# Optimization experiments

Hardware: AMD Instinct MI355X
Metric: run time of the kernel (lower is better)

The kernel has to match this reference:

```python
import jax, jax.numpy as jnp
import numpy as np

N = 10000      # nodes per graph-batch
E = 160000     # edges
G = 128        # number of graphs (segments)


def gcn_conv(x, edge_index, W, b, n):
    """PyG GCNConv with normalize=True, add_self_loops=True.
    x: [n, in], W: [in, out], b: [out], edge_index: [2, e]."""
    loops = jnp.arange(n, dtype=edge_index.dtype)
    src = jnp.concatenate([edge_index[0], loops])
    dst = jnp.concatenate([edge_index[1], loops])
    deg = jnp.zeros((n,), x.dtype).at[dst].add(1.0)          # in-degree incl. self-loops
    dinv = jnp.where(deg > 0, jax.lax.rsqrt(deg), 0.0)
    norm = dinv[src] * dinv[dst]                              # [e+n]
    h = x @ W                                                 # dense transform first
    out = jax.ops.segment_sum(norm[:, None] * h[src], dst, num_segments=n)
    return out + b


def global_max_pool(z, batch, g):
    p = jax.ops.segment_max(z, batch, num_segments=g)
    return jnp.where(jnp.isneginf(p), 0.0, p)  # guard empty segments


def setup_inputs() -> dict:
    key = jax.random.key(0)
    ks = jax.random.split(key, 24)

    def w(k, i, o):
        return (jax.random.normal(k, (i, o), jnp.float32) / np.sqrt(i)).astype(jnp.float32)

    inp = {
        "x_s": jax.random.normal(ks[0], (N, 128), jnp.float32),
        "x_t": jax.random.normal(ks[1], (N, 128), jnp.float32),
        "edge_index_s": jax.random.randint(ks[2], (2, E), 0, N, dtype=jnp.int32),
        "edge_index_t": jax.random.randint(ks[3], (2, E), 0, N, dtype=jnp.int32),
        "xs_batch": jnp.sort(jax.random.randint(ks[4], (N,), 0, G, dtype=jnp.int32)),
        "xt_batch": jnp.sort(jax.random.randint(ks[5], (N,), 0, G, dtype=jnp.int32)),
        # encoder GCNConvs (128 -> 512)
        "W_enc1": w(ks[6], 128, 512), "b_enc1": jnp.zeros((512,), jnp.float32),
        "W_enc2": w(ks[7], 128, 512), "b_enc2": jnp.zeros((512,), jnp.float32),
        # branch-1 GCNConvs
        "W_r1g1": w(ks[8], 512, 1024), "b_r1g1": jnp.zeros((1024,), jnp.float32),
        "W_r1g2": w(ks[9], 1024, 2048), "b_r1g2": jnp.zeros((2048,), jnp.float32),
        # branch-2 GCNConvs
        "W_r2g1": w(ks[10], 512, 1024), "b_r2g1": jnp.zeros((1024,), jnp.float32),
        "W_r2g2": w(ks[11], 1024, 2048), "b_r2g2": jnp.zeros((2048,), jnp.float32),
        # MLP head
        "W_l1": w(ks[12], 2048, 1024), "b_l1": jnp.zeros((1024,), jnp.float32),
        "W_l2": w(ks[13], 1024, 1317), "b_l2": jnp.zeros((1317,), jnp.float32),
    }
    return inp


def reference(x_s, x_t, W_enc1, b_enc1, W_enc2, b_enc2,
              W_r1g1, b_r1g1, W_r1g2, b_r1g2,
              W_r2g1, b_r2g1, W_r2g2, b_r2g2,
              W_l1, b_l1, W_l2, b_l2,
              edge_index_s, edge_index_t, xs_batch, xt_batch):
    # branch 1 (source graphs)
    enc_r1 = gcn_conv(x_s, edge_index_s, W_enc1, b_enc1, N)
    z_r1 = jax.nn.relu(gcn_conv(enc_r1, edge_index_s, W_r1g1, b_r1g1, N))
    z_r1 = jax.nn.relu(gcn_conv(z_r1, edge_index_s, W_r1g2, b_r1g2, N))
    # branch 2 (target graphs)
    enc_r2 = gcn_conv(x_t, edge_index_t, W_enc2, b_enc2, N)
    z_r2 = jax.nn.relu(gcn_conv(enc_r2, edge_index_t, W_r2g1, b_r2g1, N))
    z_r2 = jax.nn.relu(gcn_conv(z_r2, edge_index_t, W_r2g2, b_r2g2, N))
    # global max pool per graph, then MLP head
    z = global_max_pool(z_r1, xs_batch, G) + global_max_pool(z_r2, xt_batch, G)  # [G, 2048]
    z = jax.nn.relu(z @ W_l1 + b_l1)
    z = z @ W_l2 + b_l2                                                          # [G, 1317]
    return (z, jax.nn.sigmoid(z))
```

## Files before the change

kernel.cpp:

```cpp
#include <hip/hip_runtime.h>
#include <cstdint>
#include <cstddef>


#define NN 10000
#define NNP2 10240
#define MT2 20480
#define NB2 640
#define NE 160000
#define NG 128

typedef short bf16x8 __attribute__((ext_vector_type(8)));
typedef float f32x4 __attribute__((ext_vector_type(4)));

__device__ __forceinline__ unsigned short f2bf(float x) {
  unsigned u = __float_as_uint(x);
  u += 0x7FFFu + ((u >> 16) & 1u);
  return (unsigned short)(u >> 16);
}
__device__ __forceinline__ float bf2f(unsigned short h) {
  return __uint_as_float(((unsigned)h) << 16);
}
__device__ __forceinline__ void fma4(float4& d, float s, const float4& u) {
  d.x = fmaf(s, u.x, d.x);
  d.y = fmaf(s, u.y, d.y);
  d.z = fmaf(s, u.z, d.z);
  d.w = fmaf(s, u.w, d.w);
}

#define GLOAD_LDS16(gp, lp)                                                  \
  __builtin_amdgcn_global_load_lds(                                          \
      (const __attribute__((address_space(1))) void*)(gp),                   \
      (__attribute__((address_space(3))) void*)(lp), 16, 0, 0)


__global__ void k_count2(const int* __restrict__ eis, const int* __restrict__ eit,
                         int* __restrict__ cnt) {
  int i = blockIdx.x * blockDim.x + threadIdx.x;
  if (i >= 2 * NE) return;
  int d;
  if (i < NE) d = eis[NE + i];
  else        d = eit[NE + (i - NE)] + NNP2;
  atomicAdd(&cnt[d], 1);
}

__global__ void k_scan(const int* __restrict__ cnt, int* __restrict__ row_ptr,
                       int* __restrict__ cursor, float* __restrict__ dinv) {
  __shared__ int part[256];
  __shared__ int partex[257];
  int t = threadIdx.x;
  const int n = MT2;
  const int CH = n / 256;
  int base = t * CH;
  int s = 0;
  for (int i = 0; i < CH; ++i) s += cnt[base + i];
  part[t] = s;
  __syncthreads();
  if (t == 0) {
    int acc = 0;
    for (int i = 0; i < 256; ++i) { partex[i] = acc; acc += part[i]; }
    partex[256] = acc;
  }
  __syncthreads();
  int acc = partex[t];
  for (int i = 0; i < CH; ++i) {
    int idx = base + i;
    row_ptr[idx] = acc;
    cursor[idx]  = acc;
    dinv[idx] = rsqrtf((float)cnt[idx] + 1.0f);
    acc += cnt[idx];
  }
  if (t == 255) row_ptr[n] = partex[256];
}

__global__ void k_scatter2(const int* __restrict__ eis, const int* __restrict__ eit,
                           int* __restrict__ cursor, int* __restrict__ csr_src) {
  int i = blockIdx.x * blockDim.x + threadIdx.x;
  if (i >= 2 * NE) return;
  int s, d;
  if (i < NE) { s = eis[i]; d = eis[NE + i]; }
  else { int j = i - NE; s = eit[j] + NNP2; d = eit[NE + j] + NNP2; }
  int pos = atomicAdd(&cursor[d], 1);
  csr_src[pos] = s;
}

template <int NCH, bool DUAL>
__global__ __launch_bounds__(256) void k_agg_x(
    const float* __restrict__ in0, const float* __restrict__ in1,
    unsigned short* __restrict__ Ah, unsigned short* __restrict__ Al,
    const int* __restrict__ row_ptr, const int* __restrict__ csr_src,
    const float* __restrict__ dinv) {
  constexpr int F4TOT = NCH * 8;
  const int bid = blockIdx.x;
  const int xcd = bid & 7;
  const int seq = bid >> 3;
  int chunk, nodeblk;
  if constexpr (NCH >= 8) {
    int phase = seq / NB2;
    nodeblk = seq - phase * NB2;
    chunk = phase * 8 + xcd;
  } else {
    chunk = xcd >> 1;
    nodeblk = (seq << 1) | (xcd & 1);
  }
  const int t = threadIdx.x;
  const int node = nodeblk * 32 + (t >> 3);
  const int f4 = chunk * 8 + (t & 7);

  size_t o = (size_t)node * F4TOT + f4;
  ushort4* oh = (ushort4*)Ah + o;
  ushort4* ol = (ushort4*)Al + o;
  int local = (node < NNP2) ? node : (node - NNP2);
  if (local >= NN) {
    *oh = make_ushort4(0, 0, 0, 0);
    *ol = make_ushort4(0, 0, 0, 0);
    return;
  }
  const float4* i0 = (const float4*)in0;
  const float4* i1 = (const float4*)in1;
  auto rowp = [&](int g) -> const float4* {
    if (DUAL)
      return (g < NNP2) ? (i0 + (size_t)g * F4TOT)
                        : (i1 + (size_t)(g - NNP2) * F4TOT);
    return i0 + (size_t)g * F4TOT;
  };

  float di = dinv[node];
  float sw = di * di;
  float4 v = rowp(node)[f4];
  float4 acc;
  acc.x = sw * v.x; acc.y = sw * v.y; acc.z = sw * v.z; acc.w = sw * v.w;

  const int e0 = row_ptr[node], e1 = row_ptr[node + 1];
  int e = e0;
  for (; e + 4 <= e1; e += 4) {
    int s0 = csr_src[e], s1 = csr_src[e + 1];
    int s2 = csr_src[e + 2], s3 = csr_src[e + 3];
    float4 u0 = rowp(s0)[f4];
    float4 u1 = rowp(s1)[f4];
    float4 u2 = rowp(s2)[f4];
    float4 u3 = rowp(s3)[f4];
    float w0 = dinv[s0] * di, w1 = dinv[s1] * di;
    float w2 = dinv[s2] * di, w3 = dinv[s3] * di;
    fma4(acc, w0, u0);
    fma4(acc, w1, u1);
    fma4(acc, w2, u2);
    fma4(acc, w3, u3);
  }
  for (; e < e1; ++e) {
    int s = csr_src[e];
    float4 u = rowp(s)[f4];
    fma4(acc, dinv[s] * di, u);
  }

  ushort4 h, l;
  h.x = f2bf(acc.x); l.x = f2bf(acc.x - bf2f(h.x));
  h.y = f2bf(acc.y); l.y = f2bf(acc.y - bf2f(h.y));
  h.z = f2bf(acc.z); l.z = f2bf(acc.z - bf2f(h.z));
  h.w = f2bf(acc.w); l.w = f2bf(acc.w - bf2f(h.w));
  *oh = h;
  *ol = l;
}

__global__ __launch_bounds__(256) void k_wsplit2(
    const float* __restrict__ W0, unsigned short* __restrict__ H0,
    unsigned short* __restrict__ L0,
    const float* __restrict__ W1, unsigned short* __restrict__ H1,
    unsigned short* __restrict__ L1, int K, int N) {
  const float* W = blockIdx.z ? W1 : W0;
  unsigned short* Ht = blockIdx.z ? H1 : H0;
  unsigned short* Lt = blockIdx.z ? L1 : L0;
  __shared__ float tile[32][33];
  int nb = blockIdx.x * 32, kb = blockIdx.y * 32;
  int tx = threadIdx.x & 31, ty = threadIdx.x >> 5;
#pragma unroll
  for (int r = ty; r < 32; r += 8)
    tile[r][tx] = W[(size_t)(kb + r) * N + nb + tx];
  __syncthreads();
#pragma unroll
  for (int r = ty; r < 32; r += 8) {
    float x = tile[tx][r];
    unsigned short h = f2bf(x);
    unsigned short lo = f2bf(x - bf2f(h));
    size_t o = (size_t)(nb + r) * K + kb + tx;
    Ht[o] = h;
    Lt[o] = lo;
  }
}

template <bool RELU, int GX>
__global__ __launch_bounds__(256) void k_mgemm(
    const unsigned short* __restrict__ Ah, const unsigned short* __restrict__ Al,
    const unsigned short* __restrict__ Bh_a, const unsigned short* __restrict__ Bl_a,
    const unsigned short* __restrict__ Bh_b, const unsigned short* __restrict__ Bl_b,
    const float* __restrict__ bias_a, const float* __restrict__ bias_b,
    float* __restrict__ C, int N, int K) {
  __shared__ char smem[65536];
  const int t = threadIdx.x;
  const int w = t >> 6, l = t & 63;

  const int bid = blockIdx.x;
  const int bn_ = bid & (GX - 1), bm_ = bid / GX;
  const int bm = bm_ * 128, bn = bn_ * 128;
  const bool sec = bm >= NNP2;
  const unsigned short* Bh = sec ? Bh_b : Bh_a;
  const unsigned short* Bl = sec ? Bl_b : Bl_a;
  const float* bias = sec ? bias_b : bias_a;

  const int wr = w >> 1, wc = w & 1;

  f32x4 acc[4][4] = {};

  const unsigned short* g0 = (w == 0) ? Ah : (w == 1) ? Al : (w == 2) ? Bh : Bl;
  const int rb = (w < 2) ? bm : bn;
  const unsigned short* gbase = g0 + (size_t)(rb + (l & 15)) * K + ((l >> 4) * 8);
  const int sdoff = w * 8192 + l * 16;
  const int saoff = wr * 4096 + l * 16;
  const int sboff = 16384 + wc * 4096 + l * 16;

  const int nt = K >> 5;

#define STAGE(kt, b)                                                         \
  {                                                                          \
    const unsigned short* gk = gbase + ((kt) << 5);                          \
    char* sd = smem + (b)*32768 + sdoff;                                     \
    _Pragma("unroll") for (int s = 0; s < 8; ++s)                            \
        GLOAD_LDS16(gk + (size_t)s * 16 * K, sd + s * 1024);                 \
  }

  STAGE(0, 0)

  for (int kt = 0; kt < nt; ++kt) {
    const int cur = kt & 1;
    if (kt + 1 < nt) {
      STAGE(kt + 1, cur ^ 1)
      asm volatile("s_waitcnt vmcnt(8)" ::: "memory");
    } else {
      asm volatile("s_waitcnt vmcnt(0)" ::: "memory");
    }
    __builtin_amdgcn_sched_barrier(0);
    __builtin_amdgcn_s_barrier();

    const char* sA = smem + cur * 32768 + saoff;
    const char* sB = smem + cur * 32768 + sboff;
    bf16x8 a[4][2], b[4][2];
#pragma unroll
    for (int i = 0; i < 4; ++i) {
      a[i][0] = *(const bf16x8*)(sA + i * 1024);
      a[i][1] = *(const bf16x8*)(sA + 8192 + i * 1024);
    }
#pragma unroll
    for (int j = 0; j < 4; ++j) {
      b[j][0] = *(const bf16x8*)(sB + j * 1024);
      b[j][1] = *(const bf16x8*)(sB + 8192 + j * 1024);
    }
    asm volatile("s_waitcnt lgkmcnt(0)" ::: "memory");
    __builtin_amdgcn_sched_barrier(0);
    __builtin_amdgcn_s_barrier();

    __builtin_amdgcn_s_setprio(1);
#pragma unroll
    for (int i = 0; i < 4; ++i)
#pragma unroll
      for (int j = 0; j < 4; ++j) {
        acc[i][j] = __builtin_amdgcn_mfma_f32_16x16x32_bf16(a[i][0], b[j][0], acc[i][j], 0, 0, 0);
        acc[i][j] = __builtin_amdgcn_mfma_f32_16x16x32_bf16(a[i][0], b[j][1], acc[i][j], 0, 0, 0);
        acc[i][j] = __builtin_amdgcn_mfma_f32_16x16x32_bf16(a[i][1], b[j][0], acc[i][j], 0, 0, 0);
      }
    __builtin_amdgcn_s_setprio(0);
  }
#undef STAGE

  const int r0 = bm + wr * 64 + ((l >> 4) << 2);
  const int c0 = bn + wc * 64 + (l & 15);
#pragma unroll
  for (int j = 0; j < 4; ++j) {
    const int col = c0 + j * 16;
    const float bv = bias[col];
#pragma unroll
    for (int i = 0; i < 4; ++i) {
      const int row = r0 + i * 16;
#pragma unroll
      for (int r = 0; r < 4; ++r) {
        float v = acc[i][j][r] + bv;
        if (RELU) v = fmaxf(v, 0.f);
        C[(size_t)(row + r) * N + col] = v;
      }
    }
  }
}

__global__ __launch_bounds__(512, 2) void k_mgemm3(
    const unsigned short* __restrict__ Ah, const unsigned short* __restrict__ Al,
    const unsigned short* __restrict__ Bh_a, const unsigned short* __restrict__ Bl_a,
    const unsigned short* __restrict__ Bh_b, const unsigned short* __restrict__ Bl_b,
    const float* __restrict__ bias_a, const float* __restrict__ bias_b,
    const int* __restrict__ bs, const int* __restrict__ bt,
    float* __restrict__ P2, int N, int K) {
  __shared__ char smem[131072];
  const int t = threadIdx.x;
  const int w = t >> 6, l = t & 63;
  const int bid = blockIdx.x;
  const int bn_ = bid & 7, bm_ = bid >> 3;
  const int bm = bm_ * 256, bn = bn_ * 256;
  const bool sec = bm >= NNP2;
  const unsigned short* Bh = sec ? Bh_b : Bh_a;
  const unsigned short* Bl = sec ? Bl_b : Bl_a;
  const float* bias = sec ? bias_b : bias_a;
  const int* batch = sec ? bt : bs;
  float* P2g = P2 + (sec ? (size_t)NG * 2048 : 0);
  const int lbase = bm - (sec ? NNP2 : 0);

  const int wr = w >> 2, wc = w & 3;

  f32x4 acc[8][4] = {};

  const int part = w >> 1, half = w & 1;
  const unsigned short* gmat = (part == 0) ? Ah : (part == 1) ? Al
                             : (part == 2) ? Bh : Bl;
  const int rb = ((part < 2) ? bm : bn) + half * 128;
  const unsigned short* gsbase = gmat + (size_t)(rb + (l & 15)) * K + ((l >> 4) * 8);
  const int sdoff = part * 16384 + half * 8192 + l * 16;

  const int saoff = (wr * 8) * 1024 + l * 16;
  const int sboff = 32768 + (wc * 4) * 1024 + l * 16;

  const int nt = K >> 5;

#define STAGE3(kt, b)                                                        \
  {                                                                          \
    _Pragma("unroll") for (int c = 0; c < 8; ++c)                            \
        GLOAD_LDS16(gsbase + (size_t)c * 16 * K + ((kt) << 5),               \
                    smem + (b)*65536 + sdoff + c * 1024);                    \
  }

  STAGE3(0, 0)

  for (int kt = 0; kt < nt; ++kt) {
    const int cur = kt & 1;
    if (kt + 1 < nt) {
      STAGE3(kt + 1, cur ^ 1)
      asm volatile("s_waitcnt vmcnt(8)" ::: "memory");
    } else {
      asm volatile("s_waitcnt vmcnt(0)" ::: "memory");
    }
    __builtin_amdgcn_sched_barrier(0);
    __builtin_amdgcn_s_barrier();

    const char* base = smem + cur * 65536;
    bf16x8 bh[4], blo[4], ah[8], alo[8];
#pragma unroll
    for (int j = 0; j < 4; ++j) {
      bh[j]  = *(const bf16x8*)(base + sboff + j * 1024);
      blo[j] = *(const bf16x8*)(base + sboff + 16384 + j * 1024);
    }
#pragma unroll
    for (int i = 0; i < 8; ++i) {
      ah[i]  = *(const bf16x8*)(base + saoff + i * 1024);
      alo[i] = *(const bf16x8*)(base + saoff + 16384 + i * 1024);
    }
    asm volatile("s_waitcnt lgkmcnt(0)" ::: "memory");
    __builtin_amdgcn_sched_barrier(0);
    __builtin_amdgcn_s_barrier();

    __builtin_amdgcn_s_setprio(1);
#pragma unroll
    for (int i = 0; i < 8; ++i)
#pragma unroll
      for (int j = 0; j < 4; ++j) {
        acc[i][j] = __builtin_amdgcn_mfma_f32_16x16x32_bf16(ah[i], bh[j], acc[i][j], 0, 0, 0);
        acc[i][j] = __builtin_amdgcn_mfma_f32_16x16x32_bf16(ah[i], blo[j], acc[i][j], 0, 0, 0);
        acc[i][j] = __builtin_amdgcn_mfma_f32_16x16x32_bf16(alo[i], bh[j], acc[i][j], 0, 0, 0);
      }
    __builtin_amdgcn_s_setprio(0);
  }
#undef STAGE3

  const int r0l = lbase + wr * 128 + ((l >> 4) << 2);
  const int c0 = bn + wc * 64 + (l & 15);
#pragma unroll
  for (int j = 0; j < 4; ++j) {
    const int col = c0 + j * 16;
    const float bv = bias[col];
    float* Pcol = P2g + col;
#pragma unroll
    for (int i = 0; i < 8; ++i) {
      const int rl = r0l + i * 16;
      if (rl >= NN) continue;
      float v0 = fmaxf(acc[i][j][0] + bv, 0.f);
      float v1 = fmaxf(acc[i][j][1] + bv, 0.f);
      float v2 = fmaxf(acc[i][j][2] + bv, 0.f);
      float v3 = fmaxf(acc[i][j][3] + bv, 0.f);
      if (rl + 3 < NN) {
        int g0 = batch[rl], g3 = batch[rl + 3];
        if (g0 == g3) {
          float m = fmaxf(fmaxf(v0, v1), fmaxf(v2, v3));
          atomicMax((int*)(Pcol + (size_t)g0 * 2048), __float_as_int(m));
        } else {
          int g1 = batch[rl + 1], g2 = batch[rl + 2];
          atomicMax((int*)(Pcol + (size_t)g0 * 2048), __float_as_int(v0));
          atomicMax((int*)(Pcol + (size_t)g1 * 2048), __float_as_int(v1));
          atomicMax((int*)(Pcol + (size_t)g2 * 2048), __float_as_int(v2));
          atomicMax((int*)(Pcol + (size_t)g3 * 2048), __float_as_int(v3));
        }
      } else {
        float vv[4] = {v0, v1, v2, v3};
        for (int r = 0; r < 4; ++r) {
          if (rl + r < NN) {
            int g = batch[rl + r];
            atomicMax((int*)(Pcol + (size_t)g * 2048), __float_as_int(vv[r]));
          }
        }
      }
    }
  }
}

__global__ __launch_bounds__(256) void k_gemm_sk(
    const float* __restrict__ A, const float* __restrict__ A2,
    const float* __restrict__ B,
    float* __restrict__ PART, int M, int N, int K, int KS) {
  __shared__ float As[32][64];
  __shared__ float Bs[32][64];

  int t = threadIdx.x;
  int tx = t & 15, ty = t >> 4;
  int bm = blockIdx.y * 64, bn = blockIdx.x * 64;
  int kbeg = blockIdx.z * KS, kend = kbeg + KS;

  float acc[4][4] = {};

  int arow0 = t >> 3;
  int ak4 = (t & 7) * 4;
  int brow0 = t >> 4;
  int bn4 = (t & 15) * 4;
  const bool n4al = (N & 3) == 0;

  for (int k0 = kbeg; k0 < kend; k0 += 32) {
#pragma unroll
    for (int c = 0; c < 2; ++c) {
      int row = arow0 + c * 32;
      int gr = bm + row;
      float4 v = make_float4(0.f, 0.f, 0.f, 0.f);
      if (gr < M) {
        v = *(const float4*)&A[(size_t)gr * K + k0 + ak4];
        if (A2) {
          float4 v2 = *(const float4*)&A2[(size_t)gr * K + k0 + ak4];
          v.x += v2.x; v.y += v2.y; v.z += v2.z; v.w += v2.w;
        }
      }
      As[ak4 + 0][row] = v.x;
      As[ak4 + 1][row] = v.y;
      As[ak4 + 2][row] = v.z;
      As[ak4 + 3][row] = v.w;
    }
#pragma unroll
    for (int c = 0; c < 2; ++c) {
      int row = brow0 + c * 16;
      int gc = bn + bn4;
      const float* bp = &B[(size_t)(k0 + row) * N + gc];
      float4 v;
      if (n4al && gc + 3 < N) {
        v = *(const float4*)bp;
      } else {
        v = make_float4(0.f, 0.f, 0.f, 0.f);
        if (gc < N) v.x = bp[0];
        if (gc + 1 < N) v.y = bp[1];
        if (gc + 2 < N) v.z = bp[2];
        if (gc + 3 < N) v.w = bp[3];
      }
      *(float4*)&Bs[row][bn4] = v;
    }
    __syncthreads();

#pragma unroll
    for (int kk = 0; kk < 32; ++kk) {
      float4 a = *(const float4*)&As[kk][ty * 4];
      float4 b = *(const float4*)&Bs[kk][tx * 4];
      float av[4] = {a.x, a.y, a.z, a.w};
      float bv[4] = {b.x, b.y, b.z, b.w};
#pragma unroll
      for (int i = 0; i < 4; ++i)
#pragma unroll
        for (int j = 0; j < 4; ++j)
          acc[i][j] = fmaf(av[i], bv[j], acc[i][j]);
    }
    __syncthreads();
  }

  float* P = PART + (size_t)blockIdx.z * M * N;
  int r0 = bm + ty * 4, c0 = bn + tx * 4;
#pragma unroll
  for (int i = 0; i < 4; ++i) {
    int r = r0 + i;
    if (r < M) {
#pragma unroll
      for (int j = 0; j < 4; ++j) {
        int c = c0 + j;
        if (c < N) P[(size_t)r * N + c] = acc[i][j];
      }
    }
  }
}

template <bool SIG>
__global__ void k_reduce(const float* __restrict__ PART,
                         const float* __restrict__ bias,
                         float* __restrict__ C, float* __restrict__ C2,
                         int MN, int N, int SK) {
  int i = blockIdx.x * blockDim.x + threadIdx.x;
  if (i >= MN) return;
  float s = 0.f;
  for (int z = 0; z < SK; ++z) s += PART[(size_t)z * MN + i];
  s += bias[i % N];
  if (SIG) {
    C[i] = s;
    C2[i] = 1.0f / (1.0f + __expf(-s));
  } else {
    C[i] = fmaxf(s, 0.f);
  }
}


extern "C" void kernel_launch(void* const* d_in, const int* in_sizes, int n_in,
                              void* d_out, int out_size, void* d_ws, size_t ws_size,
                              hipStream_t stream) {
  const float* x_s = (const float*)d_in[0];
  const float* x_t = (const float*)d_in[1];
  const int* ei_s = (const int*)d_in[2];
  const int* ei_t = (const int*)d_in[3];
  const int* xs_batch = (const int*)d_in[4];
  const int* xt_batch = (const int*)d_in[5];
  const float* W_enc1 = (const float*)d_in[6];
  const float* b_enc1 = (const float*)d_in[7];
  const float* W_enc2 = (const float*)d_in[8];
  const float* b_enc2 = (const float*)d_in[9];
  const float* W_r1g1 = (const float*)d_in[10];
  const float* b_r1g1 = (const float*)d_in[11];
  const float* W_r1g2 = (const float*)d_in[12];
  const float* b_r1g2 = (const float*)d_in[13];
  const float* W_r2g1 = (const float*)d_in[14];
  const float* b_r2g1 = (const float*)d_in[15];
  const float* W_r2g2 = (const float*)d_in[16];
  const float* b_r2g2 = (const float*)d_in[17];
  const float* W_l1 = (const float*)d_in[18];
  const float* b_l1 = (const float*)d_in[19];
  const float* W_l2 = (const float*)d_in[20];
  const float* b_l2 = (const float*)d_in[21];

  float* out = (float*)d_out;

  char* ws = (char*)d_ws;
  size_t off = 0;
  auto carve = [&](size_t bytes) {
    char* p = ws + off;
    off = (off + bytes + 255) & ~(size_t)255;
    return p;
  };
  float* ACT = (float*)carve((size_t)MT2 * 1024 * 4);
  unsigned short* Ah = (unsigned short*)carve((size_t)MT2 * 1024 * 2);
  unsigned short* Al = (unsigned short*)carve((size_t)MT2 * 1024 * 2);
  unsigned short* W1h_a = (unsigned short*)carve((size_t)512 * 128 * 2);
  unsigned short* W1l_a = (unsigned short*)carve((size_t)512 * 128 * 2);
  unsigned short* W1h_b = (unsigned short*)carve((size_t)512 * 128 * 2);
  unsigned short* W1l_b = (unsigned short*)carve((size_t)512 * 128 * 2);
  unsigned short* W2h_a = (unsigned short*)carve((size_t)1024 * 512 * 2);
  unsigned short* W2l_a = (unsigned short*)carve((size_t)1024 * 512 * 2);
  unsigned short* W2h_b = (unsigned short*)carve((size_t)1024 * 512 * 2);
  unsigned short* W2l_b = (unsigned short*)carve((size_t)1024 * 512 * 2);
  unsigned short* W3h_a = (unsigned short*)carve((size_t)2048 * 1024 * 2);
  unsigned short* W3l_a = (unsigned short*)carve((size_t)2048 * 1024 * 2);
  unsigned short* W3h_b = (unsigned short*)carve((size_t)2048 * 1024 * 2);
  unsigned short* W3l_b = (unsigned short*)carve((size_t)2048 * 1024 * 2);
  float* P2   = (float*)carve((size_t)2 * NG * 2048 * 4);
  float* ZZ   = (float*)carve((size_t)NG * 1024 * 4);
  float* PART = (float*)carve((size_t)16 * NG * 1024 * 4);
  float* dinv = (float*)carve((size_t)MT2 * 4);
  int* cnt     = (int*)carve((size_t)MT2 * 4);
  int* row_ptr = (int*)carve((size_t)(MT2 + 1) * 4);
  int* cursor  = (int*)carve((size_t)MT2 * 4);
  int* csr_src = (int*)carve((size_t)2 * NE * 4);
  (void)ws_size; (void)n_in; (void)in_sizes; (void)out_size;

  k_wsplit2<<<dim3(512 / 32, 128 / 32, 2), 256, 0, stream>>>(
      W_enc1, W1h_a, W1l_a, W_enc2, W1h_b, W1l_b, 128, 512);
  k_wsplit2<<<dim3(1024 / 32, 512 / 32, 2), 256, 0, stream>>>(
      W_r1g1, W2h_a, W2l_a, W_r2g1, W2h_b, W2l_b, 512, 1024);
  k_wsplit2<<<dim3(2048 / 32, 1024 / 32, 2), 256, 0, stream>>>(
      W_r1g2, W3h_a, W3l_a, W_r2g2, W3h_b, W3l_b, 1024, 2048);

  hipMemsetAsync(cnt, 0, (size_t)MT2 * 4, stream);
  k_count2<<<(2 * NE + 255) / 256, 256, 0, stream>>>(ei_s, ei_t, cnt);
  k_scan<<<1, 256, 0, stream>>>(cnt, row_ptr, cursor, dinv);
  k_scatter2<<<(2 * NE + 255) / 256, 256, 0, stream>>>(ei_s, ei_t, cursor, csr_src);

  k_agg_x<4, true><<<NB2 * 4, 256, 0, stream>>>(
      x_s, x_t, Ah, Al, row_ptr, csr_src, dinv);
  k_mgemm<false, 4><<<4 * (MT2 / 128), 256, 0, stream>>>(
      Ah, Al, W1h_a, W1l_a, W1h_b, W1l_b, b_enc1, b_enc2, ACT, 512, 128);

  k_agg_x<16, false><<<NB2 * 16, 256, 0, stream>>>(
      ACT, nullptr, Ah, Al, row_ptr, csr_src, dinv);
  k_mgemm<true, 8><<<8 * (MT2 / 128), 256, 0, stream>>>(
      Ah, Al, W2h_a, W2l_a, W2h_b, W2l_b, b_r1g1, b_r2g1, ACT, 1024, 512);

  k_agg_x<32, false><<<NB2 * 32, 256, 0, stream>>>(
      ACT, nullptr, Ah, Al, row_ptr, csr_src, dinv);
  hipMemsetAsync(P2, 0, (size_t)2 * NG * 2048 * 4, stream);
  k_mgemm3<<<8 * (MT2 / 256), 512, 0, stream>>>(
      Ah, Al, W3h_a, W3l_a, W3h_b, W3l_b, b_r1g2, b_r2g2,
      xs_batch, xt_batch, P2, 2048, 1024);

  k_gemm_sk<<<dim3(1024 / 64, 2, 16), 256, 0, stream>>>(
      P2, P2 + (size_t)NG * 2048, W_l1, PART, NG, 1024, 2048, 128);
  k_reduce<false><<<(NG * 1024 + 255) / 256, 256, 0, stream>>>(
      PART, b_l1, ZZ, nullptr, NG * 1024, 1024, 16);

  const int OUTN = 1317;
  k_gemm_sk<<<dim3((OUTN + 63) / 64, 2, 8), 256, 0, stream>>>(
      ZZ, nullptr, W_l2, PART, NG, OUTN, 1024, 128);
  k_reduce<true><<<(NG * OUTN + 255) / 256, 256, 0, stream>>>(
      PART, b_l2, out, out + (size_t)NG * OUTN, NG * OUTN, OUTN, 8);
}
```

Baseline: 770.6 us.

## Single-buffer LDS in fused GEMM+maxpool, prefetch next tile after fragment reads

Changes the k_mgemm3 LDS staging from a 128KB double buffer to a single 64KB buffer. The next K-tile's global-to-LDS load is issued only after all waves have pulled the current tile into registers, so it overlaps with the MFMA compute. This halves shared memory per block, which can allow more resident blocks, but the load is now waited on fully (vmcnt(0)) at the top of each iteration, so prefetch depth is reduced. The variable renames in the epilogue are cosmetic.

```diff
diff --git a/kernel.cpp b/kernel.cpp
--- a/kernel.cpp
+++ b/kernel.cpp
@@ -297,7 +297,7 @@
     const float* __restrict__ bias_a, const float* __restrict__ bias_b,
     const int* __restrict__ bs, const int* __restrict__ bt,
     float* __restrict__ P2, int N, int K) {
-  __shared__ char smem[131072];
+  __shared__ char smem[65536];
   const int t = threadIdx.x;
   const int w = t >> 6, l = t & 63;
   const int bid = blockIdx.x;
@@ -327,41 +327,36 @@
 
   const int nt = K >> 5;
 
-#define STAGE3(kt, b)                                                        \
+#define STAGE3(kt)                                                           \
   {                                                                          \
     _Pragma("unroll") for (int c = 0; c < 8; ++c)                            \
         GLOAD_LDS16(gsbase + (size_t)c * 16 * K + ((kt) << 5),               \
-                    smem + (b)*65536 + sdoff + c * 1024);                    \
-  }
-
-  STAGE3(0, 0)
+                    smem + sdoff + c * 1024);                                \
+  }
+
+  STAGE3(0)
 
   for (int kt = 0; kt < nt; ++kt) {
-    const int cur = kt & 1;
-    if (kt + 1 < nt) {
-      STAGE3(kt + 1, cur ^ 1)
-      asm volatile("s_waitcnt vmcnt(8)" ::: "memory");
-    } else {
-      asm volatile("s_waitcnt vmcnt(0)" ::: "memory");
-    }
+    asm volatile("s_waitcnt vmcnt(0)" ::: "memory");
     __builtin_amdgcn_sched_barrier(0);
     __builtin_amdgcn_s_barrier();
 
-    const char* base = smem + cur * 65536;
     bf16x8 bh[4], blo[4], ah[8], alo[8];
 #pragma unroll
     for (int j = 0; j < 4; ++j) {
-      bh[j]  = *(const bf16x8*)(base + sboff + j * 1024);
-      blo[j] = *(const bf16x8*)(base + sboff + 16384 + j * 1024);
+      bh[j]  = *(const bf16x8*)(smem + sboff + j * 1024);
+      blo[j] = *(const bf16x8*)(smem + sboff + 16384 + j * 1024);
     }
 #pragma unroll
     for (int i = 0; i < 8; ++i) {
-      ah[i]  = *(const bf16x8*)(base + saoff + i * 1024);
-      alo[i] = *(const bf16x8*)(base + saoff + 16384 + i * 1024);
+      ah[i]  = *(const bf16x8*)(smem + saoff + i * 1024);
+      alo[i] = *(const bf16x8*)(smem + saoff + 16384 + i * 1024);
     }
     asm volatile("s_waitcnt lgkmcnt(0)" ::: "memory");
     __builtin_amdgcn_sched_barrier(0);
     __builtin_amdgcn_s_barrier();
+
+    if (kt + 1 < nt) STAGE3(kt + 1)
 
     __builtin_amdgcn_s_setprio(1);
 #pragma unroll
@@ -392,16 +387,16 @@
       float v2 = fmaxf(acc[i][j][2] + bv, 0.f);
       float v3 = fmaxf(acc[i][j][3] + bv, 0.f);
       if (rl + 3 < NN) {
-        int g0 = batch[rl], g3 = batch[rl + 3];
-        if (g0 == g3) {
+        int g0i = batch[rl], g3i = batch[rl + 3];
+        if (g0i == g3i) {
           float m = fmaxf(fmaxf(v0, v1), fmaxf(v2, v3));
-          atomicMax((int*)(Pcol + (size_t)g0 * 2048), __float_as_int(m));
+          atomicMax((int*)(Pcol + (size_t)g0i * 2048), __float_as_int(m));
         } else {
-          int g1 = batch[rl + 1], g2 = batch[rl + 2];
-          atomicMax((int*)(Pcol + (size_t)g0 * 2048), __float_as_int(v0));
-          atomicMax((int*)(Pcol + (size_t)g1 * 2048), __float_as_int(v1));
-          atomicMax((int*)(Pcol + (size_t)g2 * 2048), __float_as_int(v2));
-          atomicMax((int*)(Pcol + (size_t)g3 * 2048), __float_as_int(v3));
+          int g1i = batch[rl + 1], g2i = batch[rl + 2];
+          atomicMax((int*)(Pcol + (size_t)g0i * 2048), __float_as_int(v0));
+          atomicMax((int*)(Pcol + (size_t)g1i * 2048), __float_as_int(v1));
+          atomicMax((int*)(Pcol + (size_t)g2i * 2048), __float_as_int(v2));
+          atomicMax((int*)(Pcol + (size_t)g3i * 2048), __float_as_int(v3));
         }
       } else {
         float vv[4] = {v0, v1, v2, v3};
```

Result: no change. 780.8 us (+1.3%).
